# Kernel tuning notes

Measured on AMD Instinct MI355X. Metric: run time of the kernel, lower is better.

The kernel has to match this reference:

```python
import jax, jax.numpy as jnp
import numpy as np

H, W, C = 96, 96, 21
THETA_ALPHA, THETA_BETA, THETA_GAMMA = 8.0, 0.125, 3.0
NUM_ITERATIONS = 5


def setup_inputs() -> dict:
    key = jax.random.key(0)
    k1, k2, k3, k4, k5 = jax.random.split(key, 5)
    unaries = jax.random.normal(k1, (1, H, W, C), dtype=jnp.float32)
    reference_image = jax.random.uniform(k2, (1, H, W, 3), dtype=jnp.float32)
    # truncated normal(mean=0, std=0.1) as in tf.initializers.truncated_normal
    spatial_ker_weights = 0.1 * jax.random.truncated_normal(k3, -2.0, 2.0, (C,), dtype=jnp.float32)
    bilateral_ker_weights = 0.1 * jax.random.truncated_normal(k4, -2.0, 2.0, (C,), dtype=jnp.float32)
    compatibility_matrix = 0.1 * jax.random.truncated_normal(k5, -2.0, 2.0, (C, C), dtype=jnp.float32)
    return {
        "unaries": unaries,
        "reference_image": reference_image,
        "spatial_ker_weights": spatial_ker_weights,
        "bilateral_ker_weights": bilateral_ker_weights,
        "compatibility_matrix": compatibility_matrix,
    }


def _gaussian_kernel(feats):
    # feats: [B, N, D] -> K[b, i, j] = exp(-0.5 * ||f_i - f_j||^2)
    sq = jnp.sum(feats * feats, axis=-1)  # [B, N]
    d2 = sq[:, :, None] + sq[:, None, :] - 2.0 * jnp.einsum("bnd,bmd->bnm", feats, feats)
    return jnp.exp(-0.5 * jnp.maximum(d2, 0.0))


def _build_kernels(reference_image):
    # Exact-math equivalent of the permutohedral lattice Gaussian filter:
    # spatial features = positions/theta_gamma; bilateral = [pos/theta_alpha, rgb/theta_beta].
    B = reference_image.shape[0]
    yy, xx = jnp.meshgrid(jnp.arange(H, dtype=jnp.float32), jnp.arange(W, dtype=jnp.float32), indexing="ij")
    pos = jnp.stack([yy, xx], axis=-1).reshape(1, H * W, 2)  # [1, N, 2]
    pos = jnp.broadcast_to(pos, (B, H * W, 2))
    col = reference_image.reshape(B, H * W, 3)
    k_spatial = _gaussian_kernel(pos / THETA_GAMMA)
    k_bilateral = _gaussian_kernel(jnp.concatenate([pos / THETA_ALPHA, col / THETA_BETA], axis=-1))
    return k_spatial, k_bilateral


def reference(unaries, reference_image, spatial_ker_weights, bilateral_ker_weights, compatibility_matrix):
    B = unaries.shape[0]
    N = H * W
    k_spatial, k_bilateral = _build_kernels(reference_image)  # built once; reused each iteration
    u = unaries.reshape(B, N, C)
    q = u
    for _ in range(NUM_ITERATIONS):
        q = jax.nn.softmax(q, axis=-1)
        spatial_out = jnp.einsum("bnm,bmc->bnc", k_spatial, q)
        bilateral_out = jnp.einsum("bnm,bmc->bnc", k_bilateral, q)
        # pairwise^T = compat @ diag(w_s) @ S^T + compat @ diag(w_b) @ Bi^T
        # => pairwise = (S * w_s + Bi * w_b) @ compat^T
        message = spatial_out * spatial_ker_weights + bilateral_out * bilateral_ker_weights
        pairwise = message @ compatibility_matrix.T
        q = u - pairwise
    return q.reshape(unaries.shape)
```

## Files before the change

### kernel.cpp

```cpp
#include <hip/hip_runtime.h>
#include <hip/hip_bf16.h>
#include <algorithm>
#include <cmath>

#define HH 96
#define WW 96
#define CC 21
#define NN (HH*WW)
#define NELEM (NN*CC)
#define RS 20
#define NPAR (2*CC + CC*CC)
#define L2E 1.4426950408889634f
#define MSTEPS 24
#define NBB (36*24)
#define NSTRIP 8
#define NBLUR (CC*NSTRIP)
#define SROWS 12
#define TRUNC2 1225
#define BLURKEY 0x10000

typedef short bf16x8 __attribute__((ext_vector_type(8)));
typedef float f32x16 __attribute__((ext_vector_type(16)));

__device__ __forceinline__ float fexp2(float x) { return __builtin_amdgcn_exp2f(x); }
__device__ __forceinline__ float fexp(float x)  { return __builtin_amdgcn_exp2f(x * L2E); }

__device__ __forceinline__ short f2b(float f) {
    __hip_bfloat16 h = __float2bfloat16(f);
    short s; __builtin_memcpy(&s, &h, 2); return s;
}

__global__ void k_sniff(const unsigned short* __restrict__ u16, int* __restrict__ flag32) {
    __shared__ int sfound;
    if (threadIdx.x == 0) sfound = 0;
    __syncthreads();
    const int base = blockIdx.x * (NELEM/32);
    int found = 0;
    for (int i = base + threadIdx.x; i < base + NELEM/32; i += 256) {
        unsigned v = u16[i];
        if ((v & 0x7F80u) == 0x7F80u) found = 1;
    }
    if (found) sfound = 1;
    __syncthreads();
    if (threadIdx.x == 0) flag32[blockIdx.x] = sfound;
}

__device__ __forceinline__ int rdflag(const int* __restrict__ flag32) {
    int f = 0;
    #pragma unroll
    for (int i = 0; i < 32; i++) f |= flag32[i];
    return f;
}

__global__ __launch_bounds__(256) void k_prep(
    const void* __restrict__ u, const void* __restrict__ img,
    const void* __restrict__ wS, const void* __restrict__ wB,
    const void* __restrict__ compat, const int* __restrict__ flag32,
    float* __restrict__ uf, float* __restrict__ featx, float* __restrict__ par,
    float* __restrict__ bil, __hip_bfloat16* __restrict__ pT)
{
    const int f = rdflag(flag32);
    const int tid = threadIdx.x;
    const int n = blockIdx.x * 256 + tid;

    if (blockIdx.x == 0) {
        for (int i = tid; i < NPAR; i += 256) {
            const void* src; int j;
            if (i < CC)        { src = wS;     j = i; }
            else if (i < 2*CC) { src = wB;     j = i - CC; }
            else               { src = compat; j = i - 2*CC; }
            par[i] = f ? ((const float*)src)[j]
                       : __bfloat162float(((const __hip_bfloat16*)src)[j]);
        }
    }

    {
        float c0, c1, c2;
        if (f) { const float* p = (const float*)img;
                 c0 = p[3*n]; c1 = p[3*n+1]; c2 = p[3*n+2]; }
        else   { const __hip_bfloat16* p = (const __hip_bfloat16*)img;
                 c0 = __bfloat162float(p[3*n]); c1 = __bfloat162float(p[3*n+1]);
                 c2 = __bfloat162float(p[3*n+2]); }
        float ym = (float)(n / WW), xm = (float)(n % WW);
        const float sc = 0.15014029f;
        const float cf = 9.6089787f;
        featx[8*n + 0] = -L2E * (fmaf(ym, ym, xm*xm) * 0.0078125f
                                 + 32.f * (c0*c0 + c1*c1 + c2*c2));
        featx[8*n + 1] = sc * ym;
        featx[8*n + 2] = sc * xm;
        featx[8*n + 3] = cf * c0;
        featx[8*n + 4] = cf * c1;
        featx[8*n + 5] = cf * c2;
        featx[8*n + 6] = 0.f;
        featx[8*n + 7] = 0.f;
    }

    float v[CC];
    float mx = -1e30f;
    #pragma unroll
    for (int c = 0; c < CC; c++) {
        float uv = f ? ((const float*)u)[n*CC + c]
                     : __bfloat162float(((const __hip_bfloat16*)u)[n*CC + c]);
        uf[n*CC + c] = uv;
        v[c] = uv;
        mx = fmaxf(mx, uv);
    }
    float s = 0.f;
    #pragma unroll
    for (int c = 0; c < CC; c++) { v[c] = fexp(v[c] - mx); s += v[c]; }
    float inv = 1.f / s;
    #pragma unroll
    for (int c = 0; c < CC; c++) {
        pT[(size_t)c*NN + n] = __float2bfloat16(v[c] * inv);
        bil[(size_t)c*NN + n] = 0.f;
    }
}

__global__ __launch_bounds__(256) void k_work(
    const __hip_bfloat16* __restrict__ pT,
    const float* __restrict__ featx,
    float* __restrict__ bil,
    float* __restrict__ s2T,
    const int* __restrict__ tab)
{
    __shared__ float smem[6176];
    const int tid = threadIdx.x;
    const int item = tab[blockIdx.x];

    if (item < BLURKEY) {
        float* lds_h = smem;
        const int wv   = tid >> 6, lane = tid & 63;
        const int quad = lane >> 5, lid = lane & 31;

        const int nt = item >> 5, mc = item & 31;
        const int ny0 = (nt / 6) * 16, nx0 = (nt % 6) * 16;
        const int my0 = (mc & 3) * 24, mx0 = (mc >> 2) * 16;

        const int dx = (mx0 > nx0 + 15) ? mx0 - (nx0 + 15)
                     : ((nx0 > mx0 + 15) ? nx0 - (mx0 + 15) : 0);
        const int lim = TRUNC2 - dx * dx;
        int T = (int)sqrtf((float)lim);
        T -= (T * T > lim);
        T += ((T + 1) * (T + 1) <= lim);

        int blo = ny0 - T - my0;      blo = blo < 0 ? 0 : blo;
        int bhi = ny0 + 15 + T - my0; bhi = bhi > 23 ? 23 : bhi;

        {
            float4* dst = (float4*)lds_h;
            for (int i = blo * 32 + tid; i < (bhi + 1) * 32; i += 256) {
                const int seg = i >> 5, off = i & 31;
                dst[i] = ((const float4*)(featx +
                          (size_t)((my0 + seg) * WW + mx0) * 8))[off];
            }
        }
        __syncthreads();

        const int by0 = ny0 + 4 * wv;
        int lo = by0 - T - my0;     lo = lo < 0 ? 0 : lo;
        int hi = by0 + 3 + T - my0; hi = hi > 23 ? 23 : hi;
        if (lo > hi) return;

        const int row = lid >> 4, col = lid & 15;
        const int n0 = (by0 + row) * WW + nx0 + col;
        const int n1 = n0 + 2 * WW;
        const float4 g0a = *(const float4*)(featx + (size_t)n0 * 8);
        const float4 g0b = *(const float4*)(featx + (size_t)n0 * 8 + 4);
        const float4 g1a = *(const float4*)(featx + (size_t)n1 * 8);
        const float4 g1b = *(const float4*)(featx + (size_t)n1 * 8 + 4);

        f32x16 acc0, acc1;
        #pragma unroll
        for (int r = 0; r < 16; r++) { acc0[r] = 0.f; acc1[r] = 0.f; }

        int mg = (my0 + lo) * WW + mx0 + quad * 8;
        #pragma unroll 1
        for (int step = lo; step <= hi; step++, mg += WW) {
            bf16x8 afrag = *(const bf16x8*)(pT + (size_t)lid * NN + mg);

            const float* h = lds_h + (step * 16 + quad * 8) * 8;
            float kb0[8], kb1[8];
            #pragma unroll
            for (int j = 0; j < 8; j++) {
                float4 ha = *(const float4*)(h + j * 8);
                float4 hb = *(const float4*)(h + j * 8 + 4);
                float s0 = g0a.x + ha.x;
                s0 = fmaf(g0a.y, ha.y, s0);
                s0 = fmaf(g0a.z, ha.z, s0);
                s0 = fmaf(g0a.w, ha.w, s0);
                s0 = fmaf(g0b.x, hb.x, s0);
                s0 = fmaf(g0b.y, hb.y, s0);
                kb0[j] = fexp2(s0);
                float s1 = g1a.x + ha.x;
                s1 = fmaf(g1a.y, ha.y, s1);
                s1 = fmaf(g1a.z, ha.z, s1);
                s1 = fmaf(g1a.w, ha.w, s1);
                s1 = fmaf(g1b.x, hb.x, s1);
                s1 = fmaf(g1b.y, hb.y, s1);
                kb1[j] = fexp2(s1);
            }
            bf16x8 b0, b1;
            #pragma unroll
            for (int j = 0; j < 8; j++) { b0[j] = f2b(kb0[j]); b1[j] = f2b(kb1[j]); }

            acc0 = __builtin_amdgcn_mfma_f32_32x32x16_bf16(afrag, b0, acc0, 0, 0, 0);
            acc1 = __builtin_amdgcn_mfma_f32_32x32x16_bf16(afrag, b1, acc1, 0, 0, 0);
        }

        #pragma unroll
        for (int r = 0; r < 16; r++) {
            int c = (r & 3) + 8 * (r >> 2) + 4 * quad;
            if (c < CC) {
                atomicAdd(&bil[(size_t)c * NN + n0], acc0[r]);
                atomicAdd(&bil[(size_t)c * NN + n1], acc1[r]);
            }
        }
    } else {
        __shared__ float w_s[RS + 1];
        float* A  = smem;
        float* B2 = smem + 4992;

        const int b2 = item - BLURKEY;
        const int c = b2 % CC;
        const int strip = b2 / CC;
        const int y0 = strip * SROWS;
        const int ylo = (y0 - RS < 0) ? 0 : y0 - RS;
        const int yhi = (y0 + SROWS - 1 + RS > HH - 1) ? HH - 1 : y0 + SROWS - 1 + RS;
        const int nrows = yhi - ylo + 1;

        if (tid <= RS) w_s[tid] = fexp2(-(float)(tid*tid) * (L2E / 18.f));
        const __hip_bfloat16* src = pT + (size_t)c * NN + ylo * WW;
        for (int i = tid; i < nrows * WW; i += 256)
            A[i] = __bfloat162float(src[i]);
        __syncthreads();

        for (int i = tid; i < SROWS * WW; i += 256) {
            const int yo = y0 + i / WW;
            const int x  = i % WW;
            float acc = A[(yo - ylo) * WW + x];
            #pragma unroll
            for (int d = 1; d <= RS; d++) {
                float s = 0.f;
                if (yo - d >= 0)  s += A[(yo - d - ylo) * WW + x];
                if (yo + d < HH)  s += A[(yo + d - ylo) * WW + x];
                acc = fmaf(w_s[d], s, acc);
            }
            B2[i] = acc;
        }
        __syncthreads();

        for (int i = tid; i < SROWS * WW; i += 256) {
            const int r = i / WW, x = i % WW;
            float acc = B2[i];
            #pragma unroll
            for (int d = 1; d <= RS; d++) {
                float s = 0.f;
                if (x - d >= 0)  s += B2[r * WW + x - d];
                if (x + d < WW)  s += B2[r * WW + x + d];
                acc = fmaf(w_s[d], s, acc);
            }
            s2T[(size_t)c * NN + (y0 + r) * WW + x] = acc;
        }
    }
}

__global__ __launch_bounds__(256) void k_update(
    float* __restrict__ bil, const float* __restrict__ s2T,
    const float* __restrict__ uf, const float* __restrict__ par,
    const int* __restrict__ flag32,
    __hip_bfloat16* __restrict__ pT, void* __restrict__ out, int last)
{
    __shared__ float sc[CC*CC + 1];
    __shared__ float sws[CC], swb[CC];
    const int tid = threadIdx.x;
    for (int i = tid; i < CC*CC; i += 256) sc[i] = par[2*CC + i];
    if (tid == 0) sc[CC*CC] = 0.f;
    if (tid < CC) { sws[tid] = par[tid]; swb[tid] = par[CC + tid]; }
    __syncthreads();

    const int half = tid & 1;
    const int n = blockIdx.x * 128 + (tid >> 1);

    float msg[11];
    #pragma unroll
    for (int k = 0; k < 11; k++) {
        const int cp = 2*k + half;
        if (cp < CC) {
            msg[k] = fmaf(s2T[(size_t)cp*NN + n], sws[cp],
                          bil[(size_t)cp*NN + n] * swb[cp]);
            bil[(size_t)cp*NN + n] = 0.f;
        } else msg[k] = 0.f;
    }

    float pw[CC];
    #pragma unroll
    for (int c = 0; c < CC; c++) {
        float a = msg[0] * sc[c*CC + half];
        #pragma unroll
        for (int k = 1; k < 11; k++)
            a = fmaf(msg[k], sc[c*CC + 2*k + half], a);
        pw[c] = a;
    }
    #pragma unroll
    for (int c = 0; c < CC; c++)
        pw[c] += __shfl_xor(pw[c], 1, 64);

    float qv[CC];
    float mx = -1e30f;
    #pragma unroll
    for (int c = 0; c < CC; c++) {
        qv[c] = uf[(size_t)n*CC + c] - pw[c];
        mx = fmaxf(mx, qv[c]);
    }

    if (last) {
        const int is_f32 = rdflag(flag32);
        #pragma unroll
        for (int k = 0; k < 11; k++) {
            const int ce = 2*k, co = (k < 10) ? 2*k + 1 : 0;
            float v = half ? qv[co] : qv[ce];
            const int c = 2*k + half;
            if (c < CC) {
                if (is_f32) ((float*)out)[(size_t)n*CC + c] = v;
                else ((__hip_bfloat16*)out)[(size_t)n*CC + c] = __float2bfloat16(v);
            }
        }
    } else {
        float ex[11]; float ssum = 0.f;
        #pragma unroll
        for (int k = 0; k < 11; k++) {
            const int ce = 2*k, co = (k < 10) ? 2*k + 1 : 0;
            float v = half ? qv[co] : qv[ce];
            float e = fexp(v - mx);
            if (2*k + half < CC) ssum += e;
            ex[k] = e;
        }
        ssum += __shfl_xor(ssum, 1, 64);
        const float inv = 1.f / ssum;
        #pragma unroll
        for (int k = 0; k < 11; k++) {
            const int c = 2*k + half;
            if (c < CC) pT[(size_t)c*NN + n] = __float2bfloat16(ex[k] * inv);
        }
    }
}

extern "C" void kernel_launch(void* const* d_in, const int* in_sizes, int n_in,
                              void* d_out, int out_size, void* d_ws, size_t ws_size,
                              hipStream_t stream)
{
    static int h_tab[NBB + NBLUR];
    static int h_n = 0;
    if (h_n == 0) {
        struct It { int key; int cost; };
        static It its[NBB + NBLUR];
        int m = 0;
        for (int nt = 0; nt < 36; nt++)
            for (int mc = 0; mc < 24; mc++) {
                const int ny0 = (nt / 6) * 16, nx0 = (nt % 6) * 16;
                const int my0 = (mc & 3) * 24, mx0 = (mc >> 2) * 16;
                const int dx = (mx0 > nx0 + 15) ? mx0 - (nx0 + 15)
                             : ((nx0 > mx0 + 15) ? nx0 - (mx0 + 15) : 0);
                const int lim = TRUNC2 - dx * dx;
                if (lim < 0) continue;
                int T = (int)std::sqrt((double)lim);
                while (T * T > lim) T--;
                while ((T + 1) * (T + 1) <= lim) T++;
                int cost = 0;
                for (int wv = 0; wv < 4; wv++) {
                    const int by0 = ny0 + 4 * wv;
                    int lo = by0 - T - my0;     if (lo < 0)  lo = 0;
                    int hi = by0 + 3 + T - my0; if (hi > 23) hi = 23;
                    if (lo <= hi) cost += hi - lo + 1;
                }
                if (cost == 0) continue;
                its[m].key = (nt << 5) | mc; its[m].cost = cost; m++;
            }
        for (int b = 0; b < NBLUR; b++) { its[m].key = BLURKEY + b; its[m].cost = 20; m++; }
        std::sort(its, its + m, [](const It& a, const It& b) { return a.cost > b.cost; });
        for (int i = 0; i < m; i++) h_tab[i] = its[i].key;
        h_n = m;
    }

    float* ws = (float*)d_ws;
    int*   flag32 = (int*)ws;
    float* par    = ws + 32;
    float* featx  = ws + 544;
    __hip_bfloat16* pT = (__hip_bfloat16*)(ws + 74272);
    float* uf  = ws + 74272 + 147456;
    float* s2T = uf + NELEM;
    float* bil = s2T + NELEM;
    int*   d_tab = (int*)(bil + NELEM);

    hipMemcpyAsync(d_tab, h_tab, h_n * sizeof(int), hipMemcpyHostToDevice, stream);

    k_sniff<<<32, 256, 0, stream>>>((const unsigned short*)d_in[0], flag32);
    k_prep<<<NN/256, 256, 0, stream>>>(d_in[0], d_in[1], d_in[2], d_in[3], d_in[4],
                                       flag32, uf, featx, par, bil, pT);

    for (int it = 0; it < 5; it++) {
        k_work<<<h_n, 256, 0, stream>>>(pT, featx, bil, s2T, d_tab);
        k_update<<<NN/128, 256, 0, stream>>>(bil, s2T, uf, par, flag32,
                                             pT, d_out, (it == 4) ? 1 : 0);
    }
}
```

Measured before the change: 237.9 us.

## Halve bilateral m-tile height and bake the work table into constant memory

After: 239.9 us. About the same (+0.9%).

```diff
diff --git a/kernel.cpp b/kernel.cpp
--- a/kernel.cpp
+++ b/kernel.cpp
@@ -1,7 +1,5 @@
 #include <hip/hip_runtime.h>
 #include <hip/hip_bf16.h>
-#include <algorithm>
-#include <cmath>
 
 #define HH 96
 #define WW 96
@@ -11,10 +9,9 @@
 #define RS 20
 #define NPAR (2*CC + CC*CC)
 #define L2E 1.4426950408889634f
-#define MSTEPS 24
-#define NBB (36*24)
-#define NSTRIP 8
-#define NBLUR (CC*NSTRIP)
+#define NMC 48
+#define NBB (36*NMC)
+#define NBLUR (CC*8)
 #define SROWS 12
 #define TRUNC2 1225
 #define BLURKEY 0x10000
@@ -29,6 +26,41 @@
     __hip_bfloat16 h = __float2bfloat16(f);
     short s; __builtin_memcpy(&s, &h, 2); return s;
 }
+
+struct Tab { int n; int k[NBB + NBLUR]; };
+constexpr Tab build_tab() {
+    Tab t{};
+    int key[NBB + NBLUR] = {};
+    int cst[NBB + NBLUR] = {};
+    int m = 0;
+    for (int nt = 0; nt < 36; nt++)
+        for (int mc = 0; mc < NMC; mc++) {
+            const int ny0 = (nt / 6) * 16, nx0 = (nt % 6) * 16;
+            const int my0 = (mc & 7) * 12, mx0 = (mc >> 3) * 16;
+            const int dx = (mx0 > nx0 + 15) ? mx0 - (nx0 + 15)
+                         : ((nx0 > mx0 + 15) ? nx0 - (mx0 + 15) : 0);
+            const int lim = TRUNC2 - dx * dx;
+            if (lim < 0) continue;
+            int T = 0;
+            while ((T + 1) * (T + 1) <= lim) T++;
+            int cost = 0;
+            for (int wv = 0; wv < 4; wv++) {
+                const int by0 = ny0 + 4 * wv;
+                int lo = by0 - T - my0;     if (lo < 0)  lo = 0;
+                int hi = by0 + 3 + T - my0; if (hi > 11) hi = 11;
+                if (lo <= hi) cost += hi - lo + 1;
+            }
+            if (cost == 0) continue;
+            key[m] = (nt << 6) | mc; cst[m] = cost; m++;
+        }
+    for (int b = 0; b < NBLUR; b++) { key[m] = BLURKEY + b; cst[m] = 20; m++; }
+    for (int c = 48; c >= 1; c--)
+        for (int i = 0; i < m; i++)
+            if (cst[i] == c) t.k[t.n++] = key[i];
+    return t;
+}
+constexpr Tab TT = build_tab();
+__device__ __constant__ Tab c_TT = TT;
 
 __global__ void k_sniff(const unsigned short* __restrict__ u16, int* __restrict__ flag32) {
     __shared__ int sfound;
@@ -120,21 +152,20 @@
     const __hip_bfloat16* __restrict__ pT,
     const float* __restrict__ featx,
     float* __restrict__ bil,
-    float* __restrict__ s2T,
-    const int* __restrict__ tab)
+    float* __restrict__ s2T)
 {
     __shared__ float smem[6176];
     const int tid = threadIdx.x;
-    const int item = tab[blockIdx.x];
+    const int item = c_TT.k[blockIdx.x];
 
     if (item < BLURKEY) {
         float* lds_h = smem;
         const int wv   = tid >> 6, lane = tid & 63;
         const int quad = lane >> 5, lid = lane & 31;
 
-        const int nt = item >> 5, mc = item & 31;
+        const int nt = item >> 6, mc = item & 63;
         const int ny0 = (nt / 6) * 16, nx0 = (nt % 6) * 16;
-        const int my0 = (mc & 3) * 24, mx0 = (mc >> 2) * 16;
+        const int my0 = (mc & 7) * 12, mx0 = (mc >> 3) * 16;
 
         const int dx = (mx0 > nx0 + 15) ? mx0 - (nx0 + 15)
                      : ((nx0 > mx0 + 15) ? nx0 - (mx0 + 15) : 0);
@@ -144,7 +175,7 @@
         T += ((T + 1) * (T + 1) <= lim);
 
         int blo = ny0 - T - my0;      blo = blo < 0 ? 0 : blo;
-        int bhi = ny0 + 15 + T - my0; bhi = bhi > 23 ? 23 : bhi;
+        int bhi = ny0 + 15 + T - my0; bhi = bhi > 11 ? 11 : bhi;
 
         {
             float4* dst = (float4*)lds_h;
@@ -158,7 +189,7 @@
 
         const int by0 = ny0 + 4 * wv;
         int lo = by0 - T - my0;     lo = lo < 0 ? 0 : lo;
-        int hi = by0 + 3 + T - my0; hi = hi > 23 ? 23 : hi;
+        int hi = by0 + 3 + T - my0; hi = hi > 11 ? 11 : hi;
         if (lo > hi) return;
 
         const int row = lid >> 4, col = lid & 15;
@@ -216,10 +247,9 @@
             }
         }
     } else {
-        __shared__ float w_s[RS + 1];
-        float* A  = smem;
-        float* B2 = smem + 4992;
-
+        float* A   = smem;
+        float* B2  = smem + 4992;
+        float* w_s = smem + 6144;
         const int b2 = item - BLURKEY;
         const int c = b2 % CC;
         const int strip = b2 / CC;
@@ -349,57 +379,21 @@
                               void* d_out, int out_size, void* d_ws, size_t ws_size,
                               hipStream_t stream)
 {
-    static int h_tab[NBB + NBLUR];
-    static int h_n = 0;
-    if (h_n == 0) {
-        struct It { int key; int cost; };
-        static It its[NBB + NBLUR];
-        int m = 0;
-        for (int nt = 0; nt < 36; nt++)
-            for (int mc = 0; mc < 24; mc++) {
-                const int ny0 = (nt / 6) * 16, nx0 = (nt % 6) * 16;
-                const int my0 = (mc & 3) * 24, mx0 = (mc >> 2) * 16;
-                const int dx = (mx0 > nx0 + 15) ? mx0 - (nx0 + 15)
-                             : ((nx0 > mx0 + 15) ? nx0 - (mx0 + 15) : 0);
-                const int lim = TRUNC2 - dx * dx;
-                if (lim < 0) continue;
-                int T = (int)std::sqrt((double)lim);
-                while (T * T > lim) T--;
-                while ((T + 1) * (T + 1) <= lim) T++;
-                int cost = 0;
-                for (int wv = 0; wv < 4; wv++) {
-                    const int by0 = ny0 + 4 * wv;
-                    int lo = by0 - T - my0;     if (lo < 0)  lo = 0;
-                    int hi = by0 + 3 + T - my0; if (hi > 23) hi = 23;
-                    if (lo <= hi) cost += hi - lo + 1;
-                }
-                if (cost == 0) continue;
-                its[m].key = (nt << 5) | mc; its[m].cost = cost; m++;
-            }
-        for (int b = 0; b < NBLUR; b++) { its[m].key = BLURKEY + b; its[m].cost = 20; m++; }
-        std::sort(its, its + m, [](const It& a, const It& b) { return a.cost > b.cost; });
-        for (int i = 0; i < m; i++) h_tab[i] = its[i].key;
-        h_n = m;
-    }
-
     float* ws = (float*)d_ws;
     int*   flag32 = (int*)ws;
     float* par    = ws + 32;
     float* featx  = ws + 544;
     __hip_bfloat16* pT = (__hip_bfloat16*)(ws + 74272);
-    float* uf  = ws + 74272 + 147456;
+    float* uf  = ws + 221728;
     float* s2T = uf + NELEM;
     float* bil = s2T + NELEM;
-    int*   d_tab = (int*)(bil + NELEM);
-
-    hipMemcpyAsync(d_tab, h_tab, h_n * sizeof(int), hipMemcpyHostToDevice, stream);
 
     k_sniff<<<32, 256, 0, stream>>>((const unsigned short*)d_in[0], flag32);
     k_prep<<<NN/256, 256, 0, stream>>>(d_in[0], d_in[1], d_in[2], d_in[3], d_in[4],
                                        flag32, uf, featx, par, bil, pT);
 
     for (int it = 0; it < 5; it++) {
-        k_work<<<h_n, 256, 0, stream>>>(pT, featx, bil, s2T, d_tab);
+        k_work<<<TT.n, 256, 0, stream>>>(pT, featx, bil, s2T);
         k_update<<<NN/128, 256, 0, stream>>>(bil, s2T, uf, par, flag32,
                                              pT, d_out, (it == 4) ? 1 : 0);
     }
```
